# Optimization experiments

Measured on AMD Instinct MI355X. Metric: run time of the kernel, lower is better.

Reference implementation:

```python
import jax, jax.numpy as jnp
import numpy as np
import math

D_MODEL = 512
N_HEADS = 8
C = 1

def setup_inputs() -> dict:
    key = jax.random.key(0)
    ks = jax.random.split(key, 7)
    B, L, D = 4, 2048, 512
    f = lambda k, s: jax.random.normal(k, s, dtype=jnp.float32)
    return {
        "queries": f(ks[0], (B, L, D)),
        "keys": f(ks[1], (B, L, D)),
        "values": f(ks[2], (B, L, D)),
        "wq": f(ks[3], (D, D_MODEL)) * (1.0 / math.sqrt(D)),
        "wk": f(ks[4], (D, D_MODEL)) * (1.0 / math.sqrt(D)),
        "wv": f(ks[5], (D, D_MODEL)) * (1.0 / math.sqrt(D)),
        "wo": f(ks[6], (D_MODEL, D_MODEL)) * (1.0 / math.sqrt(D_MODEL)),
    }

def reference(queries, keys, values, wq, wk, wv, wo):
    B, Lq, _ = queries.shape
    Lk = keys.shape[1]
    H = N_HEADS
    Dh = D_MODEL // N_HEADS
    # projections -> [B,H,L,Dh]
    Q = (queries @ wq).reshape(B, Lq, H, Dh).transpose(0, 2, 1, 3)
    K = (keys @ wk).reshape(B, Lk, H, Dh).transpose(0, 2, 1, 3)
    V = (values @ wv).reshape(B, Lk, H, Dh).transpose(0, 2, 1, 3)
    # NOTE: original computes rfft/irfft correlation then OVERWRITES it with
    # this dense einsum; FFT branch is dead code and omitted here.
    corr = jnp.einsum('bhid,bhjd->bhij', Q, K)  # [B,H,Lq,Lk]
    # k derived from values.shape[3] == d_head in the original (quirk preserved)
    k = max(1, min(int(C * math.log(Dh)), Dh))
    mean_corr = corr.mean(axis=(1, 2))  # [B, Lk]
    top_vals, top_idx = jax.lax.top_k(mean_corr, k)  # [B,k]
    w = jax.nn.softmax(top_vals, axis=-1)  # [B,k]
    # rolled[b,j,h,l,d] = V[b,h,(l + delay[b,j]) % Lk, d]  (tf.roll with shift=-delay)
    idx = (jnp.arange(Lk)[None, None, :] + top_idx[:, :, None]) % Lk  # [B,k,Lk]
    gathered = jnp.take_along_axis(V[:, None], idx[:, :, None, :, None], axis=3)  # [B,k,H,Lk,Dh]
    agg = jnp.einsum('bk,bkhld->bhld', w, gathered)  # [B,H,Lk,Dh]
    # original: transpose (0,3,1,2) then reshape -> [B, Lq, d_model]
    out = agg.transpose(0, 3, 1, 2).reshape(B, Lq, D_MODEL)
    return out @ wo
```

## Files before the change

kernel.cpp:

```cpp
#include <hip/hip_runtime.h>
#include <hip/hip_bf16.h>
#include <float.h>
#include <math.h>

#define B  4
#define L  2048
#define D  512
#define K4 4
#define QCH 32

typedef __attribute__((ext_vector_type(8))) short  bf16x8;
typedef __attribute__((ext_vector_type(4))) float  f32x4;

#define VMIXB_OFF  0u
#define TT_OFF     8388608u
#define WVT_OFF    16777216u
#define WOT_OFF    17301504u
#define QPART_OFF  17825792u
#define TPART_OFF  18087936u
#define U_OFF      18153472u
#define SC_OFF     18161664u
#define W_OFF      18194432u
#define I_OFF      18194496u

static __device__ __forceinline__ unsigned short f2b(float f) {
    __hip_bfloat16 h = __float2bfloat16(f);
    return *reinterpret_cast<unsigned short*>(&h);
}

__global__ void k_qpart(const float* __restrict__ q, float* __restrict__ qpart) {
    int b = blockIdx.x, dc = blockIdx.y, lc = blockIdx.z;
    int d = dc * 256 + threadIdx.x;
    const float* p = q + ((size_t)b * L + (size_t)lc * (L / QCH)) * D + d;
    float acc = 0.f;
#pragma unroll 4
    for (int l = 0; l < L / QCH; ++l) acc += p[(size_t)l * D];
    qpart[((b * QCH) + lc) * D + d] = acc;
}

__global__ void k_wt(const float* __restrict__ wv, const float* __restrict__ wo,
                     unsigned short* __restrict__ wvT, unsigned short* __restrict__ woT) {
    __shared__ float s[32][33];
    const float* src = (blockIdx.z == 0) ? wv : wo;
    unsigned short* dst = (blockIdx.z == 0) ? wvT : woT;
    int c0 = blockIdx.x * 32, n0 = blockIdx.y * 32;
    int tid = threadIdx.x, col = tid & 31, r8 = tid >> 5;
#pragma unroll
    for (int rr = 0; rr < 4; ++rr) {
        int r = rr * 8 + r8;
        s[r][col] = src[(size_t)(c0 + r) * D + n0 + col];
    }
    __syncthreads();
#pragma unroll
    for (int rr = 0; rr < 4; ++rr) {
        int r = rr * 8 + r8;
        dst[(size_t)(n0 + r) * D + c0 + col] = f2b(s[col][r]);
    }
}

__global__ void k_tpart(const float* __restrict__ wq, const float* __restrict__ qpart,
                        float* __restrict__ tpart) {
    __shared__ float part[256];
    __shared__ float qs[64];
    int b = blockIdx.x, jc = blockIdx.y, tid = threadIdx.x;
    int jj = tid & 63, cg = tid >> 6;
    float p = 0.f;
#pragma unroll
    for (int c = cg * 8; c < cg * 8 + 8; ++c)
        p += qpart[((b * QCH) + c) * D + jc * 64 + jj];
    part[tid] = p;
    __syncthreads();
    if (tid < 64) qs[tid] = part[tid] + part[tid + 64] + part[tid + 128] + part[tid + 192];
    __syncthreads();
    float a0 = 0.f, a1 = 0.f;
#pragma unroll 8
    for (int j = 0; j < 64; ++j) {
        const float* wr = wq + (size_t)(jc * 64 + j) * D;
        float qv = qs[j];
        a0 += wr[tid] * qv;
        a1 += wr[tid + 256] * qv;
    }
    tpart[((b * 8) + jc) * D + tid] = a0;
    tpart[((b * 8) + jc) * D + tid + 256] = a1;
}

__global__ void k_uvec(const float* __restrict__ wk, const float* __restrict__ tpart,
                       float* __restrict__ u) {
    __shared__ float ts[D];
    int b = blockIdx.x, tid = threadIdx.x;
    for (int d = tid; d < D; d += 256) {
        float s = 0.f;
#pragma unroll
        for (int c = 0; c < 8; ++c) s += tpart[((b * 8) + c) * D + d];
        ts[d] = s;
    }
    __syncthreads();
    int wave = tid >> 6, lane = tid & 63;
#pragma unroll
    for (int rr = 0; rr < 4; ++rr) {
        int row = blockIdx.y * 16 + wave * 4 + rr;
        float acc = 0.f;
#pragma unroll
        for (int k = 0; k < 8; ++k) acc += wk[(size_t)row * D + lane + 64 * k] * ts[lane + 64 * k];
        for (int m = 32; m; m >>= 1) acc += __shfl_xor(acc, m, 64);
        if (lane == 0) u[b * D + row] = acc * (1.f / 16384.f);
    }
}

__global__ void k_scores(const float* __restrict__ keys, const float* __restrict__ u,
                         float* __restrict__ sc) {
    __shared__ float us[D];
    int b = blockIdx.x, tid = threadIdx.x;
    for (int d = tid; d < D; d += 256) us[d] = u[b * D + d];
    __syncthreads();
    int wave = tid >> 6, lane = tid & 63;
    int j = blockIdx.y * 4 + wave;
    const float* kp = keys + ((size_t)b * L + j) * D;
    float acc = 0.f;
#pragma unroll
    for (int k = 0; k < 8; ++k) acc += kp[lane + 64 * k] * us[lane + 64 * k];
    for (int m = 32; m; m >>= 1) acc += __shfl_xor(acc, m, 64);
    if (lane == 0) sc[b * L + j] = acc;
}

__global__ void k_top4(const float* __restrict__ sc, float* __restrict__ wout,
                       int* __restrict__ iout) {
    __shared__ float sv[L];
    __shared__ float rv[256];
    __shared__ int ri[256];
    __shared__ float topv[K4];
    __shared__ int topi[K4];
    int b = blockIdx.x, tid = threadIdx.x;
    for (int i = tid; i < L; i += 256) sv[i] = sc[b * L + i];
    __syncthreads();
    for (int it = 0; it < K4; ++it) {
        float bv = -FLT_MAX;
        int bi = L;
        for (int i = 0; i < L / 256; ++i) {
            int idx = tid + i * 256;
            float v = sv[idx];
            if (v > bv) { bv = v; bi = idx; }
        }
        rv[tid] = bv; ri[tid] = bi;
        __syncthreads();
        for (int off = 128; off > 0; off >>= 1) {
            if (tid < off) {
                float v2 = rv[tid + off]; int i2 = ri[tid + off];
                if (v2 > rv[tid] || (v2 == rv[tid] && i2 < ri[tid])) { rv[tid] = v2; ri[tid] = i2; }
            }
            __syncthreads();
        }
        if (tid == 0) { topv[it] = rv[0]; topi[it] = ri[0]; sv[ri[0]] = -FLT_MAX; }
        __syncthreads();
    }
    if (tid == 0) {
        float mx = topv[0];
        for (int i = 1; i < K4; ++i) mx = fmaxf(mx, topv[i]);
        float s = 0.f, e[K4];
        for (int i = 0; i < K4; ++i) { e[i] = expf(topv[i] - mx); s += e[i]; }
        for (int i = 0; i < K4; ++i) { wout[b * K4 + i] = e[i] / s; iout[b * K4 + i] = topi[i]; }
    }
}

__global__ void k_vmixb(const float* __restrict__ values, const float* __restrict__ wb,
                        const int* __restrict__ ib, uint4* __restrict__ vmixb) {
    __shared__ float wsh[K4];
    __shared__ int ish[K4];
    size_t t = (size_t)blockIdx.x * 256 + threadIdx.x;
    int b = (int)(t >> 17);
    if (threadIdx.x < K4) { wsh[threadIdx.x] = wb[b * K4 + threadIdx.x]; ish[threadIdx.x] = ib[b * K4 + threadIdx.x]; }
    __syncthreads();
    int l  = (int)((t >> 6) & (L - 1));
    int g8 = (int)(t & 63);
    const float4* vp = (const float4*)values;
    float4 r0 = make_float4(0.f, 0.f, 0.f, 0.f), r1 = r0;
#pragma unroll
    for (int j = 0; j < K4; ++j) {
        int ls = (l + ish[j]) & (L - 1);
        const float4* p = vp + ((size_t)b * L + ls) * 128 + g8 * 2;
        float4 x0 = p[0], x1 = p[1];
        float w = wsh[j];
        r0.x += w * x0.x; r0.y += w * x0.y; r0.z += w * x0.z; r0.w += w * x0.w;
        r1.x += w * x1.x; r1.y += w * x1.y; r1.z += w * x1.z; r1.w += w * x1.w;
    }
    uint4 o;
    o.x = (unsigned)f2b(r0.x) | ((unsigned)f2b(r0.y) << 16);
    o.y = (unsigned)f2b(r0.z) | ((unsigned)f2b(r0.w) << 16);
    o.z = (unsigned)f2b(r1.x) | ((unsigned)f2b(r1.y) << 16);
    o.w = (unsigned)f2b(r1.z) | ((unsigned)f2b(r1.w) << 16);
    vmixb[t] = o;
}

__global__ __launch_bounds__(256) void k_gemm1(const unsigned short* __restrict__ A,
                                               const unsigned short* __restrict__ Bt,
                                               unsigned short* __restrict__ Tt) {
    __shared__ __align__(16) unsigned short As[128][40];
    __shared__ __align__(16) unsigned short Bs[128][40];
    int m0 = blockIdx.x * 128, n0 = blockIdx.y * 128;
    int tid = threadIdx.x;
    int wave = tid >> 6, lane = tid & 63;
    int wr = wave >> 1, wc = wave & 1;
    int lg = lane >> 4, lr = lane & 15;
    f32x4 acc[4][4];
#pragma unroll
    for (int i = 0; i < 4; ++i)
#pragma unroll
        for (int j = 0; j < 4; ++j) acc[i][j] = (f32x4){0.f, 0.f, 0.f, 0.f};

    int row = tid >> 2, kc = tid & 3;
    for (int k0 = 0; k0 < D; k0 += 32) {
        uint4 va0 = *(const uint4*)(A  + (size_t)(m0 + row)      * D + k0 + kc * 8);
        uint4 va1 = *(const uint4*)(A  + (size_t)(m0 + 64 + row) * D + k0 + kc * 8);
        uint4 vb0 = *(const uint4*)(Bt + (size_t)(n0 + row)      * D + k0 + kc * 8);
        uint4 vb1 = *(const uint4*)(Bt + (size_t)(n0 + 64 + row) * D + k0 + kc * 8);
        *(uint4*)&As[row][kc * 8] = va0;
        *(uint4*)&As[64 + row][kc * 8] = va1;
        *(uint4*)&Bs[row][kc * 8] = vb0;
        *(uint4*)&Bs[64 + row][kc * 8] = vb1;
        __syncthreads();
        bf16x8 a[4], b[4];
#pragma unroll
        for (int i = 0; i < 4; ++i) a[i] = *(const bf16x8*)&As[wr * 64 + i * 16 + lr][lg * 8];
#pragma unroll
        for (int j = 0; j < 4; ++j) b[j] = *(const bf16x8*)&Bs[wc * 64 + j * 16 + lr][lg * 8];
#pragma unroll
        for (int i = 0; i < 4; ++i)
#pragma unroll
            for (int j = 0; j < 4; ++j)
                acc[i][j] = __builtin_amdgcn_mfma_f32_16x16x32_bf16(a[i], b[j], acc[i][j], 0, 0, 0);
        __syncthreads();
    }
    int bb = m0 >> 11;
#pragma unroll
    for (int i = 0; i < 4; ++i) {
        int lp = ((m0 + wr * 64 + i * 16 + lg * 4) & (L - 1));
#pragma unroll
        for (int j = 0; j < 4; ++j) {
            int cn = n0 + wc * 64 + j * 16 + lr;
            uint2 pk;
            pk.x = (unsigned)f2b(acc[i][j][0]) | ((unsigned)f2b(acc[i][j][1]) << 16);
            pk.y = (unsigned)f2b(acc[i][j][2]) | ((unsigned)f2b(acc[i][j][3]) << 16);
            *(uint2*)&Tt[((size_t)bb * D + cn) * L + lp] = pk;
        }
    }
}

__global__ __launch_bounds__(256) void k_gemm2(const unsigned short* __restrict__ Tt,
                                               const unsigned short* __restrict__ Bt,
                                               float* __restrict__ out) {
    __shared__ __align__(16) unsigned short As[128][40];
    __shared__ __align__(16) unsigned short Bs[128][40];
    int m0 = blockIdx.x * 128, n0 = blockIdx.y * 128;
    int bs = blockIdx.z;
    int bb = bs >> 2, s = bs & 3;
    const unsigned short* Ab = Tt + (size_t)bb * D * L + (size_t)s * 512;
    int tid = threadIdx.x;
    int wave = tid >> 6, lane = tid & 63;
    int wr = wave >> 1, wc = wave & 1;
    int lg = lane >> 4, lr = lane & 15;
    f32x4 acc[4][4];
#pragma unroll
    for (int i = 0; i < 4; ++i)
#pragma unroll
        for (int j = 0; j < 4; ++j) acc[i][j] = (f32x4){0.f, 0.f, 0.f, 0.f};

    int row = tid >> 2, kc = tid & 3;
    for (int k0 = 0; k0 < D; k0 += 32) {
        uint4 va0 = *(const uint4*)(Ab + (size_t)(m0 + row)      * L + k0 + kc * 8);
        uint4 va1 = *(const uint4*)(Ab + (size_t)(m0 + 64 + row) * L + k0 + kc * 8);
        uint4 vb0 = *(const uint4*)(Bt + (size_t)(n0 + row)      * D + k0 + kc * 8);
        uint4 vb1 = *(const uint4*)(Bt + (size_t)(n0 + 64 + row) * D + k0 + kc * 8);
        *(uint4*)&As[row][kc * 8] = va0;
        *(uint4*)&As[64 + row][kc * 8] = va1;
        *(uint4*)&Bs[row][kc * 8] = vb0;
        *(uint4*)&Bs[64 + row][kc * 8] = vb1;
        __syncthreads();
        bf16x8 a[4], b[4];
#pragma unroll
        for (int i = 0; i < 4; ++i) a[i] = *(const bf16x8*)&As[wr * 64 + i * 16 + lr][lg * 8];
#pragma unroll
        for (int j = 0; j < 4; ++j) b[j] = *(const bf16x8*)&Bs[wc * 64 + j * 16 + lr][lg * 8];
#pragma unroll
        for (int i = 0; i < 4; ++i)
#pragma unroll
            for (int j = 0; j < 4; ++j)
                acc[i][j] = __builtin_amdgcn_mfma_f32_16x16x32_bf16(a[i], b[j], acc[i][j], 0, 0, 0);
        __syncthreads();
    }
#pragma unroll
    for (int i = 0; i < 4; ++i) {
#pragma unroll
        for (int j = 0; j < 4; ++j) {
            int n = n0 + wc * 64 + j * 16 + lr;
#pragma unroll
            for (int r = 0; r < 4; ++r) {
                int m = m0 + wr * 64 + i * 16 + lg * 4 + r;
                int rr = ((m & 63) << 5) | ((m >> 6) << 2) | s;
                out[((size_t)bb * L + rr) * D + n] = acc[i][j][r];
            }
        }
    }
}

extern "C" void kernel_launch(void* const* d_in, const int* in_sizes, int n_in,
                              void* d_out, int out_size, void* d_ws, size_t ws_size,
                              hipStream_t stream) {
    const float* queries = (const float*)d_in[0];
    const float* keys    = (const float*)d_in[1];
    const float* values  = (const float*)d_in[2];
    const float* wq      = (const float*)d_in[3];
    const float* wk      = (const float*)d_in[4];
    const float* wv      = (const float*)d_in[5];
    const float* wo      = (const float*)d_in[6];
    float* out = (float*)d_out;
    char* ws = (char*)d_ws;

    unsigned short* vmixb = (unsigned short*)(ws + VMIXB_OFF);
    unsigned short* Tt    = (unsigned short*)(ws + TT_OFF);
    unsigned short* wvT   = (unsigned short*)(ws + WVT_OFF);
    unsigned short* woT   = (unsigned short*)(ws + WOT_OFF);
    float* qpart = (float*)(ws + QPART_OFF);
    float* tpart = (float*)(ws + TPART_OFF);
    float* u     = (float*)(ws + U_OFF);
    float* sc    = (float*)(ws + SC_OFF);
    float* wbuf  = (float*)(ws + W_OFF);
    int*   ibuf  = (int*)(ws + I_OFF);

    k_qpart<<<dim3(B, 2, QCH), 256, 0, stream>>>(queries, qpart);
    k_wt<<<dim3(16, 16, 2), 256, 0, stream>>>(wv, wo, wvT, woT);
    k_tpart<<<dim3(B, 8), 256, 0, stream>>>(wq, qpart, tpart);
    k_uvec<<<dim3(B, 32), 256, 0, stream>>>(wk, tpart, u);
    k_scores<<<dim3(B, 512), 256, 0, stream>>>(keys, u, sc);
    k_top4<<<B, 256, 0, stream>>>(sc, wbuf, ibuf);
    k_vmixb<<<2048, 256, 0, stream>>>(values, wbuf, ibuf, (uint4*)vmixb);
    k_gemm1<<<dim3(64, 4), 256, 0, stream>>>(vmixb, wvT, Tt);
    k_gemm2<<<dim3(4, 4, 16), 256, 0, stream>>>(Tt, woT, out);
}
```

Before: 75.93 us.

## Merge projection-vector kernels, vectorize reductions, double-buffer GEMMs with narrower tiles

Fuses the two small wq/wk matrix-vector kernels into one 512-thread kernel per batch, eliminating the tpart buffer and one launch. The query column-sum and key scoring now use float4 loads. Top-4 selection uses wave shuffles in place of a shared-memory tree reduction. Both MFMA GEMMs shrink their N tile to 64, doubling the block count, and double-buffer LDS so the next K-slice's global loads overlap the current MFMAs. The risk is that the fused k_tu runs only 4 blocks serially over 512x512 weights twice, which could lengthen that stage.

```diff
diff --git a/kernel.cpp b/kernel.cpp
--- a/kernel.cpp
+++ b/kernel.cpp
@@ -7,7 +7,6 @@
 #define L  2048
 #define D  512
 #define K4 4
-#define QCH 32
 
 typedef __attribute__((ext_vector_type(8))) short  bf16x8;
 typedef __attribute__((ext_vector_type(4))) float  f32x4;
@@ -17,11 +16,10 @@
 #define WVT_OFF    16777216u
 #define WOT_OFF    17301504u
 #define QPART_OFF  17825792u
-#define TPART_OFF  18087936u
-#define U_OFF      18153472u
-#define SC_OFF     18161664u
-#define W_OFF      18194432u
-#define I_OFF      18194496u
+#define U_OFF      18350080u
+#define SC_OFF     18358272u
+#define W_OFF      18391040u
+#define I_OFF      18391104u
 
 static __device__ __forceinline__ unsigned short f2b(float f) {
     __hip_bfloat16 h = __float2bfloat16(f);
@@ -29,13 +27,16 @@
 }
 
 __global__ void k_qpart(const float* __restrict__ q, float* __restrict__ qpart) {
-    int b = blockIdx.x, dc = blockIdx.y, lc = blockIdx.z;
-    int d = dc * 256 + threadIdx.x;
-    const float* p = q + ((size_t)b * L + (size_t)lc * (L / QCH)) * D + d;
-    float acc = 0.f;
-#pragma unroll 4
-    for (int l = 0; l < L / QCH; ++l) acc += p[(size_t)l * D];
-    qpart[((b * QCH) + lc) * D + d] = acc;
+    int b = blockIdx.x, lc = blockIdx.y;
+    int c4 = threadIdx.x & 127, half = threadIdx.x >> 7;
+    const float4* p = (const float4*)q + ((size_t)b * L + lc * 64 + half * 32) * 128 + c4;
+    float4 a = make_float4(0.f, 0.f, 0.f, 0.f);
+#pragma unroll 8
+    for (int l = 0; l < 32; ++l) {
+        float4 x = p[(size_t)l * 128];
+        a.x += x.x; a.y += x.y; a.z += x.z; a.w += x.w;
+    }
+    ((float4*)qpart)[((b * 64) + lc * 2 + half) * 128 + c4] = a;
 }
 
 __global__ void k_wt(const float* __restrict__ wv, const float* __restrict__ wo,
@@ -58,67 +59,50 @@
     }
 }
 
-__global__ void k_tpart(const float* __restrict__ wq, const float* __restrict__ qpart,
-                        float* __restrict__ tpart) {
-    __shared__ float part[256];
-    __shared__ float qs[64];
-    int b = blockIdx.x, jc = blockIdx.y, tid = threadIdx.x;
-    int jj = tid & 63, cg = tid >> 6;
-    float p = 0.f;
-#pragma unroll
-    for (int c = cg * 8; c < cg * 8 + 8; ++c)
-        p += qpart[((b * QCH) + c) * D + jc * 64 + jj];
-    part[tid] = p;
-    __syncthreads();
-    if (tid < 64) qs[tid] = part[tid] + part[tid + 64] + part[tid + 128] + part[tid + 192];
-    __syncthreads();
-    float a0 = 0.f, a1 = 0.f;
+__global__ __launch_bounds__(512) void k_tu(const float* __restrict__ wq, const float* __restrict__ wk,
+                                            const float* __restrict__ qpart, float* __restrict__ u) {
+    __shared__ __align__(16) float qs[D];
+    __shared__ __align__(16) float ts[D];
+    int b = blockIdx.x, tid = threadIdx.x;
+    float s = 0.f;
 #pragma unroll 8
-    for (int j = 0; j < 64; ++j) {
-        const float* wr = wq + (size_t)(jc * 64 + j) * D;
-        float qv = qs[j];
-        a0 += wr[tid] * qv;
-        a1 += wr[tid + 256] * qv;
-    }
-    tpart[((b * 8) + jc) * D + tid] = a0;
-    tpart[((b * 8) + jc) * D + tid + 256] = a1;
-}
-
-__global__ void k_uvec(const float* __restrict__ wk, const float* __restrict__ tpart,
-                       float* __restrict__ u) {
-    __shared__ float ts[D];
-    int b = blockIdx.x, tid = threadIdx.x;
-    for (int d = tid; d < D; d += 256) {
-        float s = 0.f;
-#pragma unroll
-        for (int c = 0; c < 8; ++c) s += tpart[((b * 8) + c) * D + d];
-        ts[d] = s;
-    }
-    __syncthreads();
-    int wave = tid >> 6, lane = tid & 63;
-#pragma unroll
-    for (int rr = 0; rr < 4; ++rr) {
-        int row = blockIdx.y * 16 + wave * 4 + rr;
-        float acc = 0.f;
-#pragma unroll
-        for (int k = 0; k < 8; ++k) acc += wk[(size_t)row * D + lane + 64 * k] * ts[lane + 64 * k];
+    for (int c = 0; c < 64; ++c) s += qpart[((b * 64) + c) * D + tid];
+    qs[tid] = s;
+    __syncthreads();
+    float a0 = 0.f;
+#pragma unroll 4
+    for (int j = 0; j < D; ++j) a0 += wq[(size_t)j * D + tid] * qs[j];
+    ts[tid] = a0;
+    __syncthreads();
+    int wave = tid >> 6, lane = tid & 63;
+    const float4* wk4 = (const float4*)wk;
+    float4 t0 = *(const float4*)&ts[lane * 4];
+    float4 t1 = *(const float4*)&ts[256 + lane * 4];
+    for (int r = 0; r < 64; ++r) {
+        int i = wave * 64 + r;
+        float4 w0 = wk4[(size_t)i * 128 + lane];
+        float4 w1 = wk4[(size_t)i * 128 + 64 + lane];
+        float acc = w0.x * t0.x + w0.y * t0.y + w0.z * t0.z + w0.w * t0.w
+                  + w1.x * t1.x + w1.y * t1.y + w1.z * t1.z + w1.w * t1.w;
         for (int m = 32; m; m >>= 1) acc += __shfl_xor(acc, m, 64);
-        if (lane == 0) u[b * D + row] = acc * (1.f / 16384.f);
+        if (lane == 0) u[b * D + i] = acc * (1.f / 16384.f);
     }
 }
 
 __global__ void k_scores(const float* __restrict__ keys, const float* __restrict__ u,
                          float* __restrict__ sc) {
-    __shared__ float us[D];
+    __shared__ __align__(16) float us[D];
     int b = blockIdx.x, tid = threadIdx.x;
     for (int d = tid; d < D; d += 256) us[d] = u[b * D + d];
     __syncthreads();
     int wave = tid >> 6, lane = tid & 63;
     int j = blockIdx.y * 4 + wave;
-    const float* kp = keys + ((size_t)b * L + j) * D;
-    float acc = 0.f;
-#pragma unroll
-    for (int k = 0; k < 8; ++k) acc += kp[lane + 64 * k] * us[lane + 64 * k];
+    const float4* kp = (const float4*)(keys + ((size_t)b * L + j) * D);
+    float4 u0 = *(const float4*)&us[lane * 4];
+    float4 u1 = *(const float4*)&us[256 + lane * 4];
+    float4 x0 = kp[lane], x1 = kp[lane + 64];
+    float acc = x0.x * u0.x + x0.y * u0.y + x0.z * u0.z + x0.w * u0.w
+              + x1.x * u1.x + x1.y * u1.y + x1.z * u1.z + x1.w * u1.w;
     for (int m = 32; m; m >>= 1) acc += __shfl_xor(acc, m, 64);
     if (lane == 0) sc[b * L + j] = acc;
 }
@@ -126,39 +110,44 @@
 __global__ void k_top4(const float* __restrict__ sc, float* __restrict__ wout,
                        int* __restrict__ iout) {
     __shared__ float sv[L];
-    __shared__ float rv[256];
-    __shared__ int ri[256];
+    __shared__ float wv4[4];
+    __shared__ int wi4[4];
     __shared__ float topv[K4];
     __shared__ int topi[K4];
     int b = blockIdx.x, tid = threadIdx.x;
+    int wave = tid >> 6, lane = tid & 63;
     for (int i = tid; i < L; i += 256) sv[i] = sc[b * L + i];
     __syncthreads();
     for (int it = 0; it < K4; ++it) {
         float bv = -FLT_MAX;
-        int bi = L;
-        for (int i = 0; i < L / 256; ++i) {
+        int bi = 0x7fffffff;
+#pragma unroll
+        for (int i = 0; i < 8; ++i) {
             int idx = tid + i * 256;
             float v = sv[idx];
             if (v > bv) { bv = v; bi = idx; }
         }
-        rv[tid] = bv; ri[tid] = bi;
+        for (int m = 32; m; m >>= 1) {
+            float v2 = __shfl_xor(bv, m, 64);
+            int i2 = __shfl_xor(bi, m, 64);
+            if (v2 > bv || (v2 == bv && i2 < bi)) { bv = v2; bi = i2; }
+        }
+        if (lane == 0) { wv4[wave] = bv; wi4[wave] = bi; }
         __syncthreads();
-        for (int off = 128; off > 0; off >>= 1) {
-            if (tid < off) {
-                float v2 = rv[tid + off]; int i2 = ri[tid + off];
-                if (v2 > rv[tid] || (v2 == rv[tid] && i2 < ri[tid])) { rv[tid] = v2; ri[tid] = i2; }
-            }
-            __syncthreads();
-        }
-        if (tid == 0) { topv[it] = rv[0]; topi[it] = ri[0]; sv[ri[0]] = -FLT_MAX; }
+        if (tid == 0) {
+            float mv = wv4[0]; int mi = wi4[0];
+            for (int w = 1; w < 4; ++w)
+                if (wv4[w] > mv || (wv4[w] == mv && wi4[w] < mi)) { mv = wv4[w]; mi = wi4[w]; }
+            topv[it] = mv; topi[it] = mi; sv[mi] = -FLT_MAX;
+        }
         __syncthreads();
     }
     if (tid == 0) {
         float mx = topv[0];
         for (int i = 1; i < K4; ++i) mx = fmaxf(mx, topv[i]);
-        float s = 0.f, e[K4];
-        for (int i = 0; i < K4; ++i) { e[i] = expf(topv[i] - mx); s += e[i]; }
-        for (int i = 0; i < K4; ++i) { wout[b * K4 + i] = e[i] / s; iout[b * K4 + i] = topi[i]; }
+        float ssum = 0.f, e[K4];
+        for (int i = 0; i < K4; ++i) { e[i] = expf(topv[i] - mx); ssum += e[i]; }
+        for (int i = 0; i < K4; ++i) { wout[b * K4 + i] = e[i] / ssum; iout[b * K4 + i] = topi[i]; }
     }
 }
 
@@ -194,49 +183,74 @@
 __global__ __launch_bounds__(256) void k_gemm1(const unsigned short* __restrict__ A,
                                                const unsigned short* __restrict__ Bt,
                                                unsigned short* __restrict__ Tt) {
-    __shared__ __align__(16) unsigned short As[128][40];
-    __shared__ __align__(16) unsigned short Bs[128][40];
-    int m0 = blockIdx.x * 128, n0 = blockIdx.y * 128;
+    __shared__ __align__(16) unsigned short As[2][128][40];
+    __shared__ __align__(16) unsigned short Bs[2][64][40];
+    int m0 = blockIdx.x * 128, n0 = blockIdx.y * 64;
     int tid = threadIdx.x;
     int wave = tid >> 6, lane = tid & 63;
     int wr = wave >> 1, wc = wave & 1;
-    int lg = lane >> 4, lr = lane & 15;
-    f32x4 acc[4][4];
+    int lr = lane & 15, lg = lane >> 4;
+    f32x4 acc[4][2];
 #pragma unroll
     for (int i = 0; i < 4; ++i)
 #pragma unroll
-        for (int j = 0; j < 4; ++j) acc[i][j] = (f32x4){0.f, 0.f, 0.f, 0.f};
-
-    int row = tid >> 2, kc = tid & 3;
-    for (int k0 = 0; k0 < D; k0 += 32) {
-        uint4 va0 = *(const uint4*)(A  + (size_t)(m0 + row)      * D + k0 + kc * 8);
-        uint4 va1 = *(const uint4*)(A  + (size_t)(m0 + 64 + row) * D + k0 + kc * 8);
-        uint4 vb0 = *(const uint4*)(Bt + (size_t)(n0 + row)      * D + k0 + kc * 8);
-        uint4 vb1 = *(const uint4*)(Bt + (size_t)(n0 + 64 + row) * D + k0 + kc * 8);
-        *(uint4*)&As[row][kc * 8] = va0;
-        *(uint4*)&As[64 + row][kc * 8] = va1;
-        *(uint4*)&Bs[row][kc * 8] = vb0;
-        *(uint4*)&Bs[64 + row][kc * 8] = vb1;
+        for (int j = 0; j < 2; ++j) acc[i][j] = (f32x4){0.f, 0.f, 0.f, 0.f};
+
+    int aR = tid >> 1, aC = (tid & 1) * 16;
+    int bR = tid >> 2, bC = (tid & 3) * 8;
+    const unsigned short* Ap = A + (size_t)(m0 + aR) * D + aC;
+    const unsigned short* Bp = Bt + (size_t)(n0 + bR) * D + bC;
+    {
+        uint4 va0 = *(const uint4*)(Ap);
+        uint4 va1 = *(const uint4*)(Ap + 8);
+        uint4 vb  = *(const uint4*)(Bp);
+        *(uint4*)&As[0][aR][aC]     = va0;
+        *(uint4*)&As[0][aR][aC + 8] = va1;
+        *(uint4*)&Bs[0][bR][bC]     = vb;
+    }
+    __syncthreads();
+    int cur = 0;
+    for (int t = 0; t < 15; ++t) {
+        int k0 = (t + 1) * 32;
+        uint4 va0 = *(const uint4*)(Ap + k0);
+        uint4 va1 = *(const uint4*)(Ap + k0 + 8);
+        uint4 vb  = *(const uint4*)(Bp + k0);
+        bf16x8 a[4], bq[2];
+#pragma unroll
+        for (int i = 0; i < 4; ++i) a[i] = *(const bf16x8*)&As[cur][wr * 64 + i * 16 + lr][lg * 8];
+#pragma unroll
+        for (int j = 0; j < 2; ++j) bq[j] = *(const bf16x8*)&Bs[cur][wc * 32 + j * 16 + lr][lg * 8];
+#pragma unroll
+        for (int i = 0; i < 4; ++i)
+#pragma unroll
+            for (int j = 0; j < 2; ++j)
+                acc[i][j] = __builtin_amdgcn_mfma_f32_16x16x32_bf16(a[i], bq[j], acc[i][j], 0, 0, 0);
+        *(uint4*)&As[cur ^ 1][aR][aC]     = va0;
+        *(uint4*)&As[cur ^ 1][aR][aC + 8] = va1;
+        *(uint4*)&Bs[cur ^ 1][bR][bC]     = vb;
         __syncthreads();
-        bf16x8 a[4], b[4];
-#pragma unroll
-        for (int i = 0; i < 4; ++i) a[i] = *(const bf16x8*)&As[wr * 64 + i * 16 + lr][lg * 8];
-#pragma unroll
-        for (int j = 0; j < 4; ++j) b[j] = *(const bf16x8*)&Bs[wc * 64 + j * 16 + lr][lg * 8];
+        cur ^= 1;
+    }
+    {
+        bf16x8 a[4], bq[2];
+#pragma unroll
+        for (int i = 0; i < 4; ++i) a[i] = *(const bf16x8*)&As[cur][wr * 64 + i * 16 + lr][lg * 8];
+#pragma unroll
+        for (int j = 0; j < 2; ++j) bq[j] = *(const bf16x8*)&Bs[cur][wc * 32 + j * 16 + lr][lg * 8];
 #pragma unroll
         for (int i = 0; i < 4; ++i)
 #pragma unroll
-            for (int j = 0; j < 4; ++j)
-                acc[i][j] = __builtin_amdgcn_mfma_f32_16x16x32_bf16(a[i], b[j], acc[i][j], 0, 0, 0);
-        __syncthreads();
+            for (int j = 0; j < 2; ++j)
+                acc[i][j] = __builtin_amdgcn_mfma_f32_16x16x32_bf16(a[i], bq[j], acc[i][j], 0, 0, 0);
     }
     int bb = m0 >> 11;
+    int lbase = (m0 & (L - 1)) + wr * 64 + lg * 4;
 #pragma unroll
     for (int i = 0; i < 4; ++i) {
-        int lp = ((m0 + wr * 64 + i * 16 + lg * 4) & (L - 1));
-#pragma unroll
-        for (int j = 0; j < 4; ++j) {
-            int cn = n0 + wc * 64 + j * 16 + lr;
+        int lp = lbase + i * 16;
+#pragma unroll
+        for (int j = 0; j < 2; ++j) {
+            int cn = n0 + wc * 32 + j * 16 + lr;
             uint2 pk;
             pk.x = (unsigned)f2b(acc[i][j][0]) | ((unsigned)f2b(acc[i][j][1]) << 16);
             pk.y = (unsigned)f2b(acc[i][j][2]) | ((unsigned)f2b(acc[i][j][3]) << 16);
@@ -248,50 +262,74 @@
 __global__ __launch_bounds__(256) void k_gemm2(const unsigned short* __restrict__ Tt,
                                                const unsigned short* __restrict__ Bt,
                                                float* __restrict__ out) {
-    __shared__ __align__(16) unsigned short As[128][40];
-    __shared__ __align__(16) unsigned short Bs[128][40];
-    int m0 = blockIdx.x * 128, n0 = blockIdx.y * 128;
+    __shared__ __align__(16) unsigned short As[2][128][40];
+    __shared__ __align__(16) unsigned short Bs[2][64][40];
+    int m0 = blockIdx.x * 128, n0 = blockIdx.y * 64;
     int bs = blockIdx.z;
     int bb = bs >> 2, s = bs & 3;
     const unsigned short* Ab = Tt + (size_t)bb * D * L + (size_t)s * 512;
     int tid = threadIdx.x;
     int wave = tid >> 6, lane = tid & 63;
     int wr = wave >> 1, wc = wave & 1;
-    int lg = lane >> 4, lr = lane & 15;
-    f32x4 acc[4][4];
+    int lr = lane & 15, lg = lane >> 4;
+    f32x4 acc[4][2];
 #pragma unroll
     for (int i = 0; i < 4; ++i)
 #pragma unroll
-        for (int j = 0; j < 4; ++j) acc[i][j] = (f32x4){0.f, 0.f, 0.f, 0.f};
-
-    int row = tid >> 2, kc = tid & 3;
-    for (int k0 = 0; k0 < D; k0 += 32) {
-        uint4 va0 = *(const uint4*)(Ab + (size_t)(m0 + row)      * L + k0 + kc * 8);
-        uint4 va1 = *(const uint4*)(Ab + (size_t)(m0 + 64 + row) * L + k0 + kc * 8);
-        uint4 vb0 = *(const uint4*)(Bt + (size_t)(n0 + row)      * D + k0 + kc * 8);
-        uint4 vb1 = *(const uint4*)(Bt + (size_t)(n0 + 64 + row) * D + k0 + kc * 8);
-        *(uint4*)&As[row][kc * 8] = va0;
-        *(uint4*)&As[64 + row][kc * 8] = va1;
-        *(uint4*)&Bs[row][kc * 8] = vb0;
-        *(uint4*)&Bs[64 + row][kc * 8] = vb1;
+        for (int j = 0; j < 2; ++j) acc[i][j] = (f32x4){0.f, 0.f, 0.f, 0.f};
+
+    int aR = tid >> 1, aC = (tid & 1) * 16;
+    int bR = tid >> 2, bC = (tid & 3) * 8;
+    const unsigned short* Ap = Ab + (size_t)(m0 + aR) * L + aC;
+    const unsigned short* Bp = Bt + (size_t)(n0 + bR) * D + bC;
+    {
+        uint4 va0 = *(const uint4*)(Ap);
+        uint4 va1 = *(const uint4*)(Ap + 8);
+        uint4 vb  = *(const uint4*)(Bp);
+        *(uint4*)&As[0][aR][aC]     = va0;
+        *(uint4*)&As[0][aR][aC + 8] = va1;
+        *(uint4*)&Bs[0][bR][bC]     = vb;
+    }
+    __syncthreads();
+    int cur = 0;
+    for (int t = 0; t < 15; ++t) {
+        int k0 = (t + 1) * 32;
+        uint4 va0 = *(const uint4*)(Ap + k0);
+        uint4 va1 = *(const uint4*)(Ap + k0 + 8);
+        uint4 vb  = *(const uint4*)(Bp + k0);
+        bf16x8 a[4], bq[2];
+#pragma unroll
+        for (int i = 0; i < 4; ++i) a[i] = *(const bf16x8*)&As[cur][wr * 64 + i * 16 + lr][lg * 8];
+#pragma unroll
+        for (int j = 0; j < 2; ++j) bq[j] = *(const bf16x8*)&Bs[cur][wc * 32 + j * 16 + lr][lg * 8];
+#pragma unroll
+        for (int i = 0; i < 4; ++i)
+#pragma unroll
+            for (int j = 0; j < 2; ++j)
+                acc[i][j] = __builtin_amdgcn_mfma_f32_16x16x32_bf16(a[i], bq[j], acc[i][j], 0, 0, 0);
+        *(uint4*)&As[cur ^ 1][aR][aC]     = va0;
+        *(uint4*)&As[cur ^ 1][aR][aC + 8] = va1;
+        *(uint4*)&Bs[cur ^ 1][bR][bC]     = vb;
         __syncthreads();
-        bf16x8 a[4], b[4];
-#pragma unroll
-        for (int i = 0; i < 4; ++i) a[i] = *(const bf16x8*)&As[wr * 64 + i * 16 + lr][lg * 8];
-#pragma unroll
-        for (int j = 0; j < 4; ++j) b[j] = *(const bf16x8*)&Bs[wc * 64 + j * 16 + lr][lg * 8];
+        cur ^= 1;
+    }
+    {
+        bf16x8 a[4], bq[2];
+#pragma unroll
+        for (int i = 0; i < 4; ++i) a[i] = *(const bf16x8*)&As[cur][wr * 64 + i * 16 + lr][lg * 8];
+#pragma unroll
+        for (int j = 0; j < 2; ++j) bq[j] = *(const bf16x8*)&Bs[cur][wc * 32 + j * 16 + lr][lg * 8];
 #pragma unroll
         for (int i = 0; i < 4; ++i)
 #pragma unroll
-            for (int j = 0; j < 4; ++j)
-                acc[i][j] = __builtin_amdgcn_mfma_f32_16x16x32_bf16(a[i], b[j], acc[i][j], 0, 0, 0);
-        __syncthreads();
+            for (int j = 0; j < 2; ++j)
+                acc[i][j] = __builtin_amdgcn_mfma_f32_16x16x32_bf16(a[i], bq[j], acc[i][j], 0, 0, 0);
     }
 #pragma unroll
     for (int i = 0; i < 4; ++i) {
 #pragma unroll
-        for (int j = 0; j < 4; ++j) {
-            int n = n0 + wc * 64 + j * 16 + lr;
+        for (int j = 0; j < 2; ++j) {
+            int n = n0 + wc * 32 + j * 16 + lr;
 #pragma unroll
             for (int r = 0; r < 4; ++r) {
                 int m = m0 + wr * 64 + i * 16 + lg * 4 + r;
@@ -320,19 +358,17 @@
     unsigned short* wvT   = (unsigned short*)(ws + WVT_OFF);
     unsigned short* woT   = (unsigned short*)(ws + WOT_OFF);
     float* qpart = (float*)(ws + QPART_OFF);
-    float* tpart = (float*)(ws + TPART_OFF);
     float* u     = (float*)(ws + U_OFF);
     float* sc    = (float*)(ws + SC_OFF);
     float* wbuf  = (float*)(ws + W_OFF);
     int*   ibuf  = (int*)(ws + I_OFF);
 
-    k_qpart<<<dim3(B, 2, QCH), 256, 0, stream>>>(queries, qpart);
+    k_qpart<<<dim3(B, 32), 256, 0, stream>>>(queries, qpart);
     k_wt<<<dim3(16, 16, 2), 256, 0, stream>>>(wv, wo, wvT, woT);
-    k_tpart<<<dim3(B, 8), 256, 0, stream>>>(wq, qpart, tpart);
-    k_uvec<<<dim3(B, 32), 256, 0, stream>>>(wk, tpart, u);
+    k_tu<<<B, 512, 0, stream>>>(wq, wk, qpart, u);
     k_scores<<<dim3(B, 512), 256, 0, stream>>>(keys, u, sc);
     k_top4<<<B, 256, 0, stream>>>(sc, wbuf, ibuf);
     k_vmixb<<<2048, 256, 0, stream>>>(values, wbuf, ibuf, (uint4*)vmixb);
-    k_gemm1<<<dim3(64, 4), 256, 0, stream>>>(vmixb, wvT, Tt);
-    k_gemm2<<<dim3(4, 4, 16), 256, 0, stream>>>(Tt, woT, out);
-}
+    k_gemm1<<<dim3(64, 8), 256, 0, stream>>>(vmixb, wvT, Tt);
+    k_gemm2<<<dim3(4, 8, 16), 256, 0, stream>>>(Tt, woT, out);
+}
```

Result: slower. 133.0 us (+75.2%).
